# Kernel optimization log

Measured on AMD Instinct MI355X. Metric: run time of the kernel, lower is better.

The kernel has to match this reference:

```python
import jax, jax.numpy as jnp
import numpy as np

MAX_ITER = 6
M = 3
BETA = 0.8
LAM = 1e-4


def anderson_acceleration(f, z_init, max_iter=MAX_ITER, m=M, beta=BETA, lam=LAM):
    batch_size = z_init.shape[0]
    d = z_init.size // batch_size

    def step_fn(i, state):
        z, G_hist, Z_hist = state
        f_z = f(z)
        g = f_z - z
        z_flat = z.reshape(batch_size, -1)
        g_flat = g.reshape(batch_size, -1)
        # push newest residual/iterate into history slot 0
        G_hist = jnp.roll(G_hist, 1, axis=1).at[:, 0, :].set(g_flat)
        Z_hist = jnp.roll(Z_hist, 1, axis=1).at[:, 0, :].set(z_flat)

        def simple_update(_):
            return z_flat + beta * g_flat

        def anderson_update(_):
            current_g = G_hist[:, 0, :]
            prev_G = G_hist[:, 1:, :]          # [B, m-1, D]
            current_z = Z_hist[:, 0, :]
            prev_Z = Z_hist[:, 1:, :]
            DG = current_g[:, None, :] - prev_G  # [B, m-1, D]
            DZ = current_z[:, None, :] - prev_Z
            # m == 3 -> direct 2x2 regularized normal-equation solve
            gram = jnp.einsum('bkd,bld->bkl', DG, DG) + lam * jnp.eye(m - 1)[None]
            rhs = jnp.einsum('bkd,bd->bk', DG, current_g)  # [B, 2]
            a, b_ = gram[:, 0, 0], gram[:, 0, 1]
            c, d_ = gram[:, 1, 0], gram[:, 1, 1]
            det = a * d_ - b_ * c + 1e-08
            r0, r1 = rhs[:, 0], rhs[:, 1]
            gamma0 = (d_ * r0 - b_ * r1) / det
            gamma1 = (-c * r0 + a * r1) / det
            gamma = jnp.stack([gamma0, gamma1], axis=1)[:, :, None]  # [B, 2, 1]
            correction = jnp.sum(gamma * (DZ + beta * DG), axis=1)
            return z_flat + beta * current_g - correction

        z_new_flat = jax.lax.cond(i < m, simple_update, anderson_update, None)
        return (z_new_flat.reshape(z.shape), G_hist, Z_hist)

    Z_hist = jnp.zeros((batch_size, m, d), dtype=z_init.dtype)
    G_hist = jnp.zeros((batch_size, m, d), dtype=z_init.dtype)
    final = jax.lax.fori_loop(0, max_iter, step_fn, (z_init, G_hist, Z_hist))
    return final[0]


def setup_inputs() -> dict:
    key = jax.random.key(0)
    k1, k2, k3 = jax.random.split(key, 3)
    B, D = 4096, 2048
    x_input = jax.random.normal(k1, (B, D), dtype=jnp.float32)
    # scale weights for a contractive map so the fixed point is well behaved
    W_z = jax.random.normal(k2, (D, D), dtype=jnp.float32) * (0.5 / np.sqrt(D))
    W_x = jax.random.normal(k3, (D, D), dtype=jnp.float32) * (1.0 / np.sqrt(D))
    b = jnp.zeros((D,), dtype=jnp.float32)
    return {'x_input': x_input, 'W_z': W_z, 'W_x': W_x, 'b': b}


def reference(x_input, W_z, W_x, b):
    # DEQ block: f(z, x) = tanh(z @ W_z + x @ W_x + b)
    def f(z):
        return jnp.tanh(z @ W_z + x_input @ W_x + b)
    z_init = jnp.zeros_like(x_input)
    return anderson_acceleration(f, z_init)
```

## Files before the change

### kernel.cpp

```cpp
#include <hip/hip_runtime.h>

typedef __bf16 bf16x8 __attribute__((ext_vector_type(8)));
typedef float f32x4 __attribute__((ext_vector_type(4)));

#define BETA 0.8f
#define LAM 1e-4f

__device__ __forceinline__ unsigned short f2bf(float x) {
  unsigned u = __float_as_uint(x);
  u += 0x7FFFu + ((u >> 16) & 1u);
  return (unsigned short)(u >> 16);
}
__device__ __forceinline__ float bf2f(unsigned short h) {
  return __uint_as_float(((unsigned)h) << 16);
}
__device__ __forceinline__ void split2(float x, unsigned short& h, unsigned short& l) {
  h = f2bf(x);
  l = f2bf(x - bf2f(h));
}
__device__ __forceinline__ float fast_tanh(float x) {
  float e = __expf(2.0f * x);
  return 1.0f - 2.0f / (e + 1.0f);
}

__device__ __forceinline__ void async_cp16(const void* g, void* l) {
  __builtin_amdgcn_global_load_lds(
      (const __attribute__((address_space(1))) void*)g,
      (__attribute__((address_space(3))) void*)l, 16, 0, 0);
}

template<int MODE>
__global__ __launch_bounds__(256, 2)
void gemm_bf16x3(const unsigned short* __restrict__ Ahi,
                 const unsigned short* __restrict__ Alo,
                 const unsigned short* __restrict__ Bhi,
                 const unsigned short* __restrict__ Blo,
                 const float* __restrict__ addv,
                 const float* zin,
                 float* __restrict__ gout,
                 float* uout,
                 int M, int N, int K)
{
  __shared__ unsigned short As[128 * 128];
  __shared__ unsigned short Bs[128 * 128];

  const int tid    = threadIdx.x;
  const int lane   = tid & 63;
  const int w      = tid >> 6;
  const int wrow   = w >> 1, wcol = w & 1;
  const int lane15 = lane & 15;
  const int q      = lane >> 4;

  const int nwg = gridDim.x;
  const int bid = blockIdx.x;
  const int sw  = (bid & 7) * (nwg >> 3) + (bid >> 3);
  const int nby = M >> 7;
  const int by  = sw % nby;
  const int bx  = sw / nby;
  const int m0 = by * 128;
  const int n0 = bx * 128;

  const int rin   = lane >> 4;
  const int pslot = lane & 15;

  f32x4 acc[4][4];
#pragma unroll
  for (int i = 0; i < 4; ++i)
#pragma unroll
    for (int j = 0; j < 4; ++j) acc[i][j] = f32x4{0.f, 0.f, 0.f, 0.f};

  for (int kt = 0; kt < K; kt += 64) {
#pragma unroll
    for (int t = 0; t < 8; ++t) {
      int c   = t * 4 + w;
      int row = c * 4 + rin;
      int ls  = pslot ^ (row & 7);
      const unsigned short* sa = (ls < 8 ? Ahi : Alo)
          + (size_t)(m0 + row) * K + kt + (ls & 7) * 8;
      async_cp16(sa, &As[c * 512]);
      const unsigned short* sb = (ls < 8 ? Bhi : Blo)
          + (size_t)(n0 + row) * K + kt + (ls & 7) * 8;
      async_cp16(sb, &Bs[c * 512]);
    }
    __syncthreads();

#pragma unroll
    for (int s = 0; s < 2; ++s) {
      bf16x8 ah[4], al[4], bh[4], bl[4];
#pragma unroll
      for (int mi = 0; mi < 4; ++mi) {
        int r = wrow * 64 + mi * 16 + lane15;
        const char* rowp = (const char*)As + r * 256;
        int x7 = r & 7;
        int sl = (s * 4 + q) ^ x7;
        ah[mi] = *(const bf16x8*)(rowp + sl * 16);
        al[mi] = *(const bf16x8*)(rowp + (8 + sl) * 16);
      }
#pragma unroll
      for (int ni = 0; ni < 4; ++ni) {
        int r = wcol * 64 + ni * 16 + lane15;
        const char* rowp = (const char*)Bs + r * 256;
        int x7 = r & 7;
        int sl = (s * 4 + q) ^ x7;
        bh[ni] = *(const bf16x8*)(rowp + sl * 16);
        bl[ni] = *(const bf16x8*)(rowp + (8 + sl) * 16);
      }
#pragma unroll
      for (int mi = 0; mi < 4; ++mi)
#pragma unroll
        for (int ni = 0; ni < 4; ++ni) {
          acc[mi][ni] = __builtin_amdgcn_mfma_f32_16x16x32_bf16(ah[mi], bh[ni], acc[mi][ni], 0, 0, 0);
          acc[mi][ni] = __builtin_amdgcn_mfma_f32_16x16x32_bf16(ah[mi], bl[ni], acc[mi][ni], 0, 0, 0);
          acc[mi][ni] = __builtin_amdgcn_mfma_f32_16x16x32_bf16(al[mi], bh[ni], acc[mi][ni], 0, 0, 0);
        }
    }
    __syncthreads();
  }

#pragma unroll
  for (int mi = 0; mi < 4; ++mi)
#pragma unroll
    for (int ni = 0; ni < 4; ++ni)
#pragma unroll
      for (int j = 0; j < 4; ++j) {
        int m = m0 + wrow * 64 + mi * 16 + q * 4 + j;
        int n = n0 + wcol * 64 + ni * 16 + lane15;
        size_t idx = (size_t)m * N + n;
        float a = acc[mi][ni][j];
        if (MODE == 0) {
          gout[idx] = a + addv[n];
        } else {
          float zv = zin[idx];
          float v  = fast_tanh(a + addv[idx]);
          float gg = v - zv;
          gout[idx] = gg;
          uout[idx] = fmaf(BETA, gg, zv);
        }
      }
}


__global__ void split_rows_k(const float* __restrict__ X, unsigned short* __restrict__ H,
                             unsigned short* __restrict__ L, long n4)
{
  long i = (long)blockIdx.x * blockDim.x + threadIdx.x;
  long stride = (long)gridDim.x * blockDim.x;
  for (; i < n4; i += stride) {
    float4 v = ((const float4*)X)[i];
    ushort4 h, l;
    split2(v.x, h.x, l.x); split2(v.y, h.y, l.y);
    split2(v.z, h.z, l.z); split2(v.w, h.w, l.w);
    ((ushort4*)H)[i] = h; ((ushort4*)L)[i] = l;
  }
}

__global__ void split_transpose_k(const float* __restrict__ W,
                                  unsigned short* __restrict__ Th,
                                  unsigned short* __restrict__ Tl, int D)
{
  __shared__ float tile[32][33];
  int n0 = blockIdx.x * 32, k0 = blockIdx.y * 32;
  int tx = threadIdx.x, ty = threadIdx.y;
  for (int r = ty; r < 32; r += 8)
    tile[r][tx] = W[(size_t)(k0 + r) * D + n0 + tx];
  __syncthreads();
  for (int r = ty; r < 32; r += 8) {
    float v = tile[tx][r];
    unsigned short h, l; split2(v, h, l);
    size_t o = (size_t)(n0 + r) * D + k0 + tx;
    Th[o] = h; Tl[o] = l;
  }
}

__global__ void iter0_k(const float* __restrict__ Xb, float* __restrict__ u0,
                        unsigned short* __restrict__ zh,
                        unsigned short* __restrict__ zl, long n4)
{
  long i = (long)blockIdx.x * blockDim.x + threadIdx.x;
  long stride = (long)gridDim.x * blockDim.x;
  for (; i < n4; i += stride) {
    float4 xb = ((const float4*)Xb)[i];
    float4 z;
    z.x = BETA * fast_tanh(xb.x); z.y = BETA * fast_tanh(xb.y);
    z.z = BETA * fast_tanh(xb.z); z.w = BETA * fast_tanh(xb.w);
    ((float4*)u0)[i] = z;
    ushort4 h, l;
    split2(z.x, h.x, l.x); split2(z.y, h.y, l.y);
    split2(z.z, h.z, l.z); split2(z.w, h.w, l.w);
    ((ushort4*)zh)[i] = h; ((ushort4*)zl)[i] = l;
  }
}

__global__ __launch_bounds__(256) void gram_k(const float* __restrict__ g,
                                              const float* __restrict__ gm1,
                                              const float* __restrict__ gm2,
                                              float* __restrict__ gamma, int D)
{
  int row = blockIdx.x;
  const float4* G0 = (const float4*)(g   + (size_t)row * D);
  const float4* G1 = (const float4*)(gm1 + (size_t)row * D);
  const float4* G2 = (const float4*)(gm2 + (size_t)row * D);
  float s00 = 0, s01 = 0, s11 = 0, r0 = 0, r1 = 0;
  int n4 = D >> 2;
  for (int t = threadIdx.x; t < n4; t += 256) {
    float4 a = G0[t], b = G1[t], c = G2[t];
    { float gg = a.x, d0 = gg - b.x, d1 = gg - c.x;
      s00 += d0*d0; s01 += d0*d1; s11 += d1*d1; r0 += d0*gg; r1 += d1*gg; }
    { float gg = a.y, d0 = gg - b.y, d1 = gg - c.y;
      s00 += d0*d0; s01 += d0*d1; s11 += d1*d1; r0 += d0*gg; r1 += d1*gg; }
    { float gg = a.z, d0 = gg - b.z, d1 = gg - c.z;
      s00 += d0*d0; s01 += d0*d1; s11 += d1*d1; r0 += d0*gg; r1 += d1*gg; }
    { float gg = a.w, d0 = gg - b.w, d1 = gg - c.w;
      s00 += d0*d0; s01 += d0*d1; s11 += d1*d1; r0 += d0*gg; r1 += d1*gg; }
  }
  for (int off = 32; off > 0; off >>= 1) {
    s00 += __shfl_down(s00, off); s01 += __shfl_down(s01, off);
    s11 += __shfl_down(s11, off); r0 += __shfl_down(r0, off); r1 += __shfl_down(r1, off);
  }
  __shared__ float red[4][5];
  int lane = threadIdx.x & 63, wv = threadIdx.x >> 6;
  if (lane == 0) { red[wv][0]=s00; red[wv][1]=s01; red[wv][2]=s11; red[wv][3]=r0; red[wv][4]=r1; }
  __syncthreads();
  if (threadIdx.x == 0) {
    s00 = red[0][0]+red[1][0]+red[2][0]+red[3][0];
    s01 = red[0][1]+red[1][1]+red[2][1]+red[3][1];
    s11 = red[0][2]+red[1][2]+red[2][2]+red[3][2];
    r0  = red[0][3]+red[1][3]+red[2][3]+red[3][3];
    r1  = red[0][4]+red[1][4]+red[2][4]+red[3][4];
    float a_ = s00 + LAM, d_ = s11 + LAM, b_ = s01;
    float det = a_ * d_ - b_ * b_ + 1e-8f;
    gamma[row * 2]     = (d_ * r0 - b_ * r1) / det;
    gamma[row * 2 + 1] = (a_ * r1 - b_ * r0) / det;
  }
}

template<int WSPLIT>
__global__ void anderson_update_k(const float* uc, const float* um1,
                                  const float* um2, const float* __restrict__ gamma,
                                  float* zn, unsigned short* __restrict__ zh,
                                  unsigned short* __restrict__ zl, long n4, int logD4)
{
  long i = (long)blockIdx.x * blockDim.x + threadIdx.x;
  long stride = (long)gridDim.x * blockDim.x;
  for (; i < n4; i += stride) {
    long row = i >> logD4;
    float c0 = gamma[row * 2], c1 = gamma[row * 2 + 1];
    float4 u0 = ((const float4*)uc)[i];
    float4 u1 = ((const float4*)um1)[i];
    float4 u2 = ((const float4*)um2)[i];
    float4 o;
    o.x = u0.x - (c0 * (u0.x - u1.x) + c1 * (u0.x - u2.x));
    o.y = u0.y - (c0 * (u0.y - u1.y) + c1 * (u0.y - u2.y));
    o.z = u0.z - (c0 * (u0.z - u1.z) + c1 * (u0.z - u2.z));
    o.w = u0.w - (c0 * (u0.w - u1.w) + c1 * (u0.w - u2.w));
    ((float4*)zn)[i] = o;
    if (WSPLIT) {
      ushort4 h, l;
      split2(o.x, h.x, l.x); split2(o.y, h.y, l.y);
      split2(o.z, h.z, l.z); split2(o.w, h.w, l.w);
      ((ushort4*)zh)[i] = h; ((ushort4*)zl)[i] = l;
    }
  }
}


extern "C" void kernel_launch(void* const* d_in, const int* in_sizes, int n_in,
                              void* d_out, int out_size, void* d_ws, size_t ws_size,
                              hipStream_t stream)
{
  const float* x  = (const float*)d_in[0];
  const float* Wz = (const float*)d_in[1];
  const float* Wx = (const float*)d_in[2];
  const float* b  = (const float*)d_in[3];
  const int D = in_sizes[3];
  const int B = in_sizes[0] / D;
  const size_t BD = (size_t)B * D, DD = (size_t)D * D;

  float* Xb  = (float*)d_ws;
  float* gb0 = Xb + BD;
  float* gb1 = gb0 + BD;
  float* gb2 = gb1 + BD;
  float* S0  = gb2 + BD;
  float* S1  = S0 + BD;
  unsigned short* zhi = (unsigned short*)(S1 + BD);
  unsigned short* zlo = zhi + BD;
  unsigned short* Wth = zlo + BD;
  unsigned short* Wtl = Wth + DD;
  float* gamma = (float*)(Wtl + DD);

  float* S[3] = { S0, S1, (float*)d_out };
  float* gslot[3] = { gb0, gb1, gb2 };
  const int zin_i[6] = { 0, 0, 1, 2, 1, 2 };

  dim3 tblk(32, 8);
  dim3 tgrd(D / 32, D / 32);
  int ggrd = (D / 128) * (B / 128);
  long n4 = (long)(BD >> 2);
  int logD4 = 31 - __builtin_clz((unsigned)(D >> 2));
  const int ebl = 2048;

  split_transpose_k<<<tgrd, tblk, 0, stream>>>(Wx, Wth, Wtl, D);
  split_rows_k<<<ebl, 256, 0, stream>>>(x, zhi, zlo, n4);
  gemm_bf16x3<0><<<ggrd, 256, 0, stream>>>(zhi, zlo, Wth, Wtl, b, nullptr,
                                           Xb, nullptr, B, D, D);
  split_transpose_k<<<tgrd, tblk, 0, stream>>>(Wz, Wth, Wtl, D);

  iter0_k<<<ebl, 256, 0, stream>>>(Xb, S[0], zhi, zlo, n4);

  for (int i = 1; i <= 5; ++i) {
    float* zi = S[zin_i[i]];
    float* gi = gslot[i % 3];
    float* ui = S[i % 3];
    gemm_bf16x3<1><<<ggrd, 256, 0, stream>>>(zhi, zlo, Wth, Wtl, Xb, zi,
                                             gi, ui, B, D, D);
    if (i <= 2) {
      split_rows_k<<<ebl, 256, 0, stream>>>(ui, zhi, zlo, n4);
    } else {
      gram_k<<<B, 256, 0, stream>>>(gi, gslot[(i - 1) % 3], gslot[(i - 2) % 3], gamma, D);
      float* zn = (i == 5) ? (float*)d_out : S[(i + 1) % 3];
      if (i < 5)
        anderson_update_k<1><<<ebl, 256, 0, stream>>>(S[i % 3], S[(i - 1) % 3], S[(i - 2) % 3],
                                                      gamma, zn, zhi, zlo, n4, logD4);
      else
        anderson_update_k<0><<<ebl, 256, 0, stream>>>(S[i % 3], S[(i - 1) % 3], S[(i - 2) % 3],
                                                      gamma, zn, nullptr, nullptr, n4, logD4);
    }
  }
}
```

Measured before the change: 966.1 us.

## Shrink GEMM tile to 128x64 with K-step 32 and raise occupancy

Changes the bf16x3 GEMM block tile from 128x128 with K-step 64 to 128x64 with K-step 32. Shared memory per block drops, so launch bounds now allow 4 blocks per SM. The LDS loading and swizzle pattern are rewritten to match, and the grid doubles. The aim is more resident waves to hide the latency of loads and barriers, at the cost of less data reuse per tile and more barriers per unit of K.

Result: slower. 1.259 ms (+30.3%).

```diff
diff --git a/kernel.cpp b/kernel.cpp
--- a/kernel.cpp
+++ b/kernel.cpp
@@ -30,7 +30,7 @@
 }
 
 template<int MODE>
-__global__ __launch_bounds__(256, 2)
+__global__ __launch_bounds__(256, 4)
 void gemm_bf16x3(const unsigned short* __restrict__ Ahi,
                  const unsigned short* __restrict__ Alo,
                  const unsigned short* __restrict__ Bhi,
@@ -41,8 +41,8 @@
                  float* uout,
                  int M, int N, int K)
 {
-  __shared__ unsigned short As[128 * 128];
-  __shared__ unsigned short Bs[128 * 128];
+  __shared__ unsigned short As[128 * 64];
+  __shared__ unsigned short Bs[64 * 64];
 
   const int tid    = threadIdx.x;
   const int lane   = tid & 63;
@@ -58,73 +58,74 @@
   const int by  = sw % nby;
   const int bx  = sw / nby;
   const int m0 = by * 128;
-  const int n0 = bx * 128;
-
-  const int rin   = lane >> 4;
-  const int pslot = lane & 15;
-
-  f32x4 acc[4][4];
+  const int n0 = bx * 64;
+
+  const int srow8 = lane >> 3;
+  const int sslot = (lane & 7) ^ srow8;
+  const int s_hi  = (sslot < 4);
+  const int s_ko  = (sslot & 3) * 8;
+
+  f32x4 acc[4][2];
 #pragma unroll
   for (int i = 0; i < 4; ++i)
 #pragma unroll
-    for (int j = 0; j < 4; ++j) acc[i][j] = f32x4{0.f, 0.f, 0.f, 0.f};
-
-  for (int kt = 0; kt < K; kt += 64) {
-#pragma unroll
-    for (int t = 0; t < 8; ++t) {
+    for (int j = 0; j < 2; ++j) acc[i][j] = f32x4{0.f, 0.f, 0.f, 0.f};
+
+  for (int kt = 0; kt < K; kt += 32) {
+#pragma unroll
+    for (int t = 0; t < 4; ++t) {
       int c   = t * 4 + w;
-      int row = c * 4 + rin;
-      int ls  = pslot ^ (row & 7);
-      const unsigned short* sa = (ls < 8 ? Ahi : Alo)
-          + (size_t)(m0 + row) * K + kt + (ls & 7) * 8;
+      int row = c * 8 + srow8;
+      const unsigned short* sa = (s_hi ? Ahi : Alo)
+          + (size_t)(m0 + row) * K + kt + s_ko;
       async_cp16(sa, &As[c * 512]);
-      const unsigned short* sb = (ls < 8 ? Bhi : Blo)
-          + (size_t)(n0 + row) * K + kt + (ls & 7) * 8;
+    }
+#pragma unroll
+    for (int t = 0; t < 2; ++t) {
+      int c   = t * 4 + w;
+      int row = c * 8 + srow8;
+      const unsigned short* sb = (s_hi ? Bhi : Blo)
+          + (size_t)(n0 + row) * K + kt + s_ko;
       async_cp16(sb, &Bs[c * 512]);
     }
     __syncthreads();
 
-#pragma unroll
-    for (int s = 0; s < 2; ++s) {
-      bf16x8 ah[4], al[4], bh[4], bl[4];
-#pragma unroll
-      for (int mi = 0; mi < 4; ++mi) {
-        int r = wrow * 64 + mi * 16 + lane15;
-        const char* rowp = (const char*)As + r * 256;
-        int x7 = r & 7;
-        int sl = (s * 4 + q) ^ x7;
-        ah[mi] = *(const bf16x8*)(rowp + sl * 16);
-        al[mi] = *(const bf16x8*)(rowp + (8 + sl) * 16);
+    bf16x8 ah[4], al[4], bh[2], bl[2];
+#pragma unroll
+    for (int mi = 0; mi < 4; ++mi) {
+      int r = wrow * 64 + mi * 16 + lane15;
+      const char* base = (const char*)As + r * 128;
+      int swz = (r & 7) << 4;
+      ah[mi] = *(const bf16x8*)(base + ((q << 4) ^ swz));
+      al[mi] = *(const bf16x8*)(base + ((64 + (q << 4)) ^ swz));
+    }
+#pragma unroll
+    for (int ni = 0; ni < 2; ++ni) {
+      int r = wcol * 32 + ni * 16 + lane15;
+      const char* base = (const char*)Bs + r * 128;
+      int swz = (r & 7) << 4;
+      bh[ni] = *(const bf16x8*)(base + ((q << 4) ^ swz));
+      bl[ni] = *(const bf16x8*)(base + ((64 + (q << 4)) ^ swz));
+    }
+#pragma unroll
+    for (int mi = 0; mi < 4; ++mi)
+#pragma unroll
+      for (int ni = 0; ni < 2; ++ni) {
+        acc[mi][ni] = __builtin_amdgcn_mfma_f32_16x16x32_bf16(ah[mi], bh[ni], acc[mi][ni], 0, 0, 0);
+        acc[mi][ni] = __builtin_amdgcn_mfma_f32_16x16x32_bf16(ah[mi], bl[ni], acc[mi][ni], 0, 0, 0);
+        acc[mi][ni] = __builtin_amdgcn_mfma_f32_16x16x32_bf16(al[mi], bh[ni], acc[mi][ni], 0, 0, 0);
       }
-#pragma unroll
-      for (int ni = 0; ni < 4; ++ni) {
-        int r = wcol * 64 + ni * 16 + lane15;
-        const char* rowp = (const char*)Bs + r * 256;
-        int x7 = r & 7;
-        int sl = (s * 4 + q) ^ x7;
-        bh[ni] = *(const bf16x8*)(rowp + sl * 16);
-        bl[ni] = *(const bf16x8*)(rowp + (8 + sl) * 16);
-      }
-#pragma unroll
-      for (int mi = 0; mi < 4; ++mi)
-#pragma unroll
-        for (int ni = 0; ni < 4; ++ni) {
-          acc[mi][ni] = __builtin_amdgcn_mfma_f32_16x16x32_bf16(ah[mi], bh[ni], acc[mi][ni], 0, 0, 0);
-          acc[mi][ni] = __builtin_amdgcn_mfma_f32_16x16x32_bf16(ah[mi], bl[ni], acc[mi][ni], 0, 0, 0);
-          acc[mi][ni] = __builtin_amdgcn_mfma_f32_16x16x32_bf16(al[mi], bh[ni], acc[mi][ni], 0, 0, 0);
-        }
-    }
     __syncthreads();
   }
 
 #pragma unroll
   for (int mi = 0; mi < 4; ++mi)
 #pragma unroll
-    for (int ni = 0; ni < 4; ++ni)
+    for (int ni = 0; ni < 2; ++ni)
 #pragma unroll
       for (int j = 0; j < 4; ++j) {
         int m = m0 + wrow * 64 + mi * 16 + q * 4 + j;
-        int n = n0 + wcol * 64 + ni * 16 + lane15;
+        int n = n0 + wcol * 32 + ni * 16 + lane15;
         size_t idx = (size_t)m * N + n;
         float a = acc[mi][ni][j];
         if (MODE == 0) {
@@ -294,7 +295,7 @@
 
   dim3 tblk(32, 8);
   dim3 tgrd(D / 32, D / 32);
-  int ggrd = (D / 128) * (B / 128);
+  int ggrd = (B / 128) * (D / 64);
   long n4 = (long)(BD >> 2);
   int logD4 = 31 - __builtin_clz((unsigned)(D >> 2));
   const int ebl = 2048;
```
